# Optimization experiments

Measured on AMD Instinct MI355X. Metric: run time of the kernel, lower is better.

## Reference

```python
import jax, jax.numpy as jnp
import numpy as np

N = 100_000   # nodes
E = 1_600_000 # edges (avg degree 16)
D = 128       # in_dim
H = 128       # hidden_dim


def _glorot(key, shape):
    s = 1.0 / np.sqrt(shape[0])
    return jax.random.uniform(key, shape, jnp.float32, -s, s)


def setup_inputs() -> dict:
    key = jax.random.key(0)
    ks = jax.random.split(key, 8)
    x = jax.random.normal(ks[0], (N, D), jnp.float32)
    edge_index = jax.random.randint(ks[1], (2, E), 0, N)
    return {
        "x": x,
        "edge_index": edge_index,
        "Wn0": _glorot(ks[2], (D, H)),
        "Wr0": _glorot(ks[3], (D, H)),
        "b0": jnp.zeros((H,), jnp.float32),
        "Wn1": _glorot(ks[4], (H, H)),
        "Wr1": _glorot(ks[5], (H, H)),
        "b1": jnp.zeros((H,), jnp.float32),
        "Wh": _glorot(ks[6], (H, 1)),
        "bh": jnp.zeros((1,), jnp.float32),
    }


def _mean_agg(h, src, dst, n):
    # mean of source-node features scattered onto destination nodes
    summed = jax.ops.segment_sum(h[src], dst, num_segments=n)  # [N, F]
    cnt = jax.ops.segment_sum(jnp.ones((src.shape[0],), h.dtype), dst,
                              num_segments=n)
    return summed / jnp.maximum(cnt, 1.0)[:, None]


def _sage_layer(h, src, dst, Wn, Wr, b):
    # PyG SAGEConv (mean aggr): lin_l(mean_neighbors) + lin_r(root) + bias
    agg = _mean_agg(h, src, dst, h.shape[0])
    return agg @ Wn + h @ Wr + b


def reference(x, edge_index, Wn0, Wr0, b0, Wn1, Wr1, b1, Wh, bh):
    src, dst = edge_index[0], edge_index[1]
    h = jax.nn.relu(_sage_layer(x, src, dst, Wn0, Wr0, b0))  # dropout = identity (eval)
    h = jax.nn.relu(_sage_layer(h, src, dst, Wn1, Wr1, b1))
    logits = (h @ Wh + bh)[:, 0]  # squeeze(-1) -> [N]
    return logits
```

## Files before the change

### kernel.cpp

```cpp
#include <hip/hip_runtime.h>

#define THREADS 256
#define SCAN_ITEMS 8
#define NSB 128
#define BKT_MAX 3200
#define CHUNK 1024

typedef float f32x4 __attribute__((ext_vector_type(4)));
typedef __bf16 bf16x8 __attribute__((ext_vector_type(8)));
typedef int intx4 __attribute__((ext_vector_type(4)));

__device__ inline unsigned short f32_to_bf16_rne(float f) {
    unsigned int u = __float_as_uint(f);
    unsigned int r = u + 0x7fffu + ((u >> 16) & 1u);
    return (unsigned short)(r >> 16);
}
__device__ inline float bf16_bits_to_f32(unsigned short h) {
    return __uint_as_float(((unsigned int)h) << 16);
}
__device__ inline uint4 pack8(const unsigned short* s) {
    uint4 u;
    u.x = (unsigned int)s[0] | ((unsigned int)s[1] << 16);
    u.y = (unsigned int)s[2] | ((unsigned int)s[3] << 16);
    u.z = (unsigned int)s[4] | ((unsigned int)s[5] << 16);
    u.w = (unsigned int)s[6] | ((unsigned int)s[7] << 16);
    return u;
}

__global__ __launch_bounds__(256) void hist32(const int* __restrict__ dst,
                                              int* __restrict__ hist,
                                              int E, int nbkt, int chunk) {
    __shared__ int lh[BKT_MAX];
    const int tid = threadIdx.x, blk = blockIdx.x;
    for (int i = tid; i < nbkt; i += 256) lh[i] = 0;
    __syncthreads();
    int s = blk * chunk, e = s + chunk; if (e > E) e = E;
    if (((size_t)dst & 15) == 0) {
        int n4 = (e > s) ? ((e - s) >> 2) : 0;
        const intx4* d4p = (const intx4*)(dst + s);
        for (int i = tid; i < n4; i += 256) {
            intx4 d4 = d4p[i];
#pragma unroll
            for (int k = 0; k < 4; k++) atomicAdd(&lh[d4[k] >> 5], 1);
        }
        for (int j = s + (n4 << 2) + tid; j < e; j += 256) atomicAdd(&lh[dst[j] >> 5], 1);
    } else {
        for (int j = s + tid; j < e; j += 256) atomicAdd(&lh[dst[j] >> 5], 1);
    }
    __syncthreads();
    for (int i = tid; i < nbkt; i += 256) hist[i * NSB + blk] = lh[i];
}

__global__ void scan1_kernel(const int* __restrict__ cnt, int* __restrict__ off,
                             int* __restrict__ bsums, int n) {
    __shared__ int sdata[THREADS];
    int base = blockIdx.x * (THREADS * SCAN_ITEMS) + threadIdx.x * SCAN_ITEMS;
    int vals[SCAN_ITEMS];
    int tsum = 0;
#pragma unroll
    for (int k = 0; k < SCAN_ITEMS; k++) {
        int idx = base + k;
        int v = (idx < n) ? cnt[idx] : 0;
        vals[k] = tsum;
        tsum += v;
    }
    sdata[threadIdx.x] = tsum;
    __syncthreads();
    for (int s = 1; s < THREADS; s <<= 1) {
        int y = (threadIdx.x >= (unsigned)s) ? sdata[threadIdx.x - s] : 0;
        __syncthreads();
        sdata[threadIdx.x] += y;
        __syncthreads();
    }
    int texcl = sdata[threadIdx.x] - tsum;
#pragma unroll
    for (int k = 0; k < SCAN_ITEMS; k++) {
        int idx = base + k;
        if (idx < n) off[idx] = texcl + vals[k];
    }
    if (threadIdx.x == THREADS - 1) bsums[blockIdx.x] = sdata[THREADS - 1];
}

__global__ void scan2_kernel(const int* __restrict__ bsums, int* __restrict__ bbase,
                             int nb, int* __restrict__ offN) {
    if (threadIdx.x == 0 && blockIdx.x == 0) {
        int run = 0;
        for (int i = 0; i < nb; i++) { bbase[i] = run; run += bsums[i]; }
        *offN = run;
    }
}

__global__ void scan3b_kernel(int* __restrict__ off, const int* __restrict__ bbase, int n) {
    int i = blockIdx.x * blockDim.x + threadIdx.x;
    if (i < n) off[i] += bbase[i >> 11];
}

__global__ __launch_bounds__(256) void scatter32(const int* __restrict__ src,
                                                 const int* __restrict__ dst,
                                                 const int* __restrict__ hstS,
                                                 int* __restrict__ esrt,
                                                 int E, int nbkt, int chunk) {
    __shared__ int cur[BKT_MAX];
    const int tid = threadIdx.x, blk = blockIdx.x;
    for (int i = tid; i < nbkt; i += 256) cur[i] = hstS[i * NSB + blk];
    __syncthreads();
    int s = blk * chunk, e = s + chunk; if (e > E) e = E;
    if ((((size_t)dst | (size_t)src) & 15) == 0) {
        int n4 = (e > s) ? ((e - s) >> 2) : 0;
        const intx4* d4p = (const intx4*)(dst + s);
        const intx4* s4p = (const intx4*)(src + s);
        for (int i = tid; i < n4; i += 256) {
            intx4 d4 = d4p[i];
            intx4 s4 = s4p[i];
#pragma unroll
            for (int k = 0; k < 4; k++) {
                int d = d4[k];
                int p = atomicAdd(&cur[d >> 5], 1);
                esrt[p] = s4[k] | ((d & 31) << 17);
            }
        }
        for (int j = s + (n4 << 2) + tid; j < e; j += 256) {
            int d = dst[j];
            int p = atomicAdd(&cur[d >> 5], 1);
            esrt[p] = src[j] | ((d & 31) << 17);
        }
    } else {
        for (int j = s + tid; j < e; j += 256) {
            int d = dst[j];
            int p = atomicAdd(&cur[d >> 5], 1);
            esrt[p] = src[j] | ((d & 31) << 17);
        }
    }
}

__global__ void cvt_bf16_kernel(const float4* __restrict__ x, ushort4* __restrict__ o, int n4) {
    int i = blockIdx.x * blockDim.x + threadIdx.x;
    if (i < n4) {
        float4 v = x[i];
        ushort4 r;
        r.x = f32_to_bf16_rne(v.x);
        r.y = f32_to_bf16_rne(v.y);
        r.z = f32_to_bf16_rne(v.z);
        r.w = f32_to_bf16_rne(v.w);
        o[i] = r;
    }
}

__global__ void swizzle_w_kernel(const float* __restrict__ Wn, const float* __restrict__ Wr,
                                 uint4* __restrict__ out) {
    int id = blockIdx.x * blockDim.x + threadIdx.x;
    if (id >= 4096) return;
    int lane = id & 63;
    int nt = (id >> 6) & 7;
    int t = id >> 9;
    int kbase = t * 32 + (lane >> 4) * 8;
    int col = nt * 16 + (lane & 15);
    unsigned short hi[8], lo[8];
#pragma unroll
    for (int j = 0; j < 8; j++) {
        int k = kbase + j;
        const float* W = (k < 128) ? (Wn + (size_t)k * 128) : (Wr + (size_t)(k - 128) * 128);
        float v = W[col];
        unsigned short h = f32_to_bf16_rne(v);
        hi[j] = h;
        lo[j] = f32_to_bf16_rne(v - bf16_bits_to_f32(h));
    }
    out[(size_t)((t * 8 + nt) * 2 + 0) * 64 + lane] = pack8(hi);
    out[(size_t)((t * 8 + nt) * 2 + 1) * 64 + lane] = pack8(lo);
}

__global__ __launch_bounds__(256) void agg_bucket(const unsigned short* __restrict__ hb,
                                                  const int* __restrict__ hstS,
                                                  const int* __restrict__ esrt,
                                                  unsigned short* __restrict__ aggb,
                                                  int E, int nbkt, int n) {
    __shared__ int stage[CHUNK];
    __shared__ int sorted[CHUNK];
    __shared__ int cnt[32];
    __shared__ int coff[33];
    const int tid = threadIdx.x, lane = tid & 63, w = tid >> 6;
    const int b = blockIdx.x;

    const int p0 = hstS[b * NSB];
    const int p1 = (b + 1 < nbkt) ? hstS[(b + 1) * NSB] : E;

    if (p1 - p0 <= CHUNK) {
        int m = p1 - p0;
        for (int i = tid; i < m; i += 256) stage[i] = esrt[p0 + i];
        if (tid < 32) cnt[tid] = 0;
        __syncthreads();
        for (int i = tid; i < m; i += 256) atomicAdd(&cnt[(stage[i] >> 17) & 31], 1);
        __syncthreads();
        if (tid < 32) {
            int v = cnt[tid];
            int x = v;
#pragma unroll
            for (int s = 1; s < 32; s <<= 1) {
                int y = __shfl_up(x, s);
                if (lane >= s) x += y;
            }
            coff[tid + 1] = x;
            if (tid == 0) coff[0] = 0;
            cnt[tid] = x - v;
        }
        __syncthreads();
        for (int i = tid; i < m; i += 256) {
            int pk = stage[i];
            int p = atomicAdd(&cnt[(pk >> 17) & 31], 1);
            sorted[p] = pk;
        }
        __syncthreads();
        const int nodeEnd = w * 8 + 8;
        int cur = w * 8;
        int s = coff[cur], e2 = coff[nodeEnd];
        float ax = 0.f, ay = 0.f;
        int i = s;
        for (; i + 8 <= e2; i += 8) {
            unsigned int v[8];
            int nd[8];
#pragma unroll
            for (int j = 0; j < 8; j++) {
                int pk = sorted[i + j];
                nd[j] = (pk >> 17) & 31;
                v[j] = *(const unsigned int*)(hb + (size_t)(pk & 0x1FFFF) * 128 + lane * 2);
            }
#pragma unroll
            for (int j = 0; j < 8; j++) {
                while (cur < nd[j]) {
                    int node = b * 32 + cur;
                    int d = coff[cur + 1] - coff[cur];
                    float inv = 1.0f / (float)(d > 1 ? d : 1);
                    unsigned int o = (unsigned int)f32_to_bf16_rne(ax * inv)
                                   | ((unsigned int)f32_to_bf16_rne(ay * inv) << 16);
                    if (node < n)
                        *(unsigned int*)(aggb + (size_t)node * 128 + lane * 2) = o;
                    ax = 0.f; ay = 0.f; cur++;
                }
                ax += __uint_as_float(v[j] << 16);
                ay += __uint_as_float(v[j] & 0xffff0000u);
            }
        }
        for (; i < e2; i++) {
            int pk = sorted[i];
            int nd = (pk >> 17) & 31;
            unsigned int vv = *(const unsigned int*)(hb + (size_t)(pk & 0x1FFFF) * 128 + lane * 2);
            while (cur < nd) {
                int node = b * 32 + cur;
                int d = coff[cur + 1] - coff[cur];
                float inv = 1.0f / (float)(d > 1 ? d : 1);
                unsigned int o = (unsigned int)f32_to_bf16_rne(ax * inv)
                               | ((unsigned int)f32_to_bf16_rne(ay * inv) << 16);
                if (node < n)
                    *(unsigned int*)(aggb + (size_t)node * 128 + lane * 2) = o;
                ax = 0.f; ay = 0.f; cur++;
            }
            ax += __uint_as_float(vv << 16);
            ay += __uint_as_float(vv & 0xffff0000u);
        }
        while (cur < nodeEnd) {
            int node = b * 32 + cur;
            int d = coff[cur + 1] - coff[cur];
            float inv = 1.0f / (float)(d > 1 ? d : 1);
            unsigned int o = (unsigned int)f32_to_bf16_rne(ax * inv)
                           | ((unsigned int)f32_to_bf16_rne(ay * inv) << 16);
            if (node < n)
                *(unsigned int*)(aggb + (size_t)node * 128 + lane * 2) = o;
            ax = 0.f; ay = 0.f; cur++;
        }
        return;
    }

    float accx[8], accy[8];
    int dcnt[8];
#pragma unroll
    for (int nl = 0; nl < 8; nl++) { accx[nl] = 0.f; accy[nl] = 0.f; dcnt[nl] = 0; }
    for (int base = p0; base < p1; base += CHUNK) {
        int m = p1 - base; if (m > CHUNK) m = CHUNK;
        for (int i = tid; i < m; i += 256) stage[i] = esrt[base + i];
        if (tid < 32) cnt[tid] = 0;
        __syncthreads();
        for (int i = tid; i < m; i += 256) atomicAdd(&cnt[(stage[i] >> 17) & 31], 1);
        __syncthreads();
        if (tid < 32) {
            int v = cnt[tid];
            int x = v;
#pragma unroll
            for (int s = 1; s < 32; s <<= 1) {
                int y = __shfl_up(x, s);
                if (lane >= s) x += y;
            }
            coff[tid + 1] = x;
            if (tid == 0) coff[0] = 0;
            cnt[tid] = x - v;
        }
        __syncthreads();
        for (int i = tid; i < m; i += 256) {
            int pk = stage[i];
            int p = atomicAdd(&cnt[(pk >> 17) & 31], 1);
            sorted[p] = pk;
        }
        __syncthreads();
#pragma unroll
        for (int nl = 0; nl < 8; nl++) {
            int node_l = w * 8 + nl;
            int s = coff[node_l], e2 = coff[node_l + 1];
            dcnt[nl] += e2 - s;
            float ax = accx[nl], ay = accy[nl];
            int i = s;
            for (; i + 8 <= e2; i += 8) {
                unsigned int v[8];
#pragma unroll
                for (int j = 0; j < 8; j++) {
                    int sj = sorted[i + j] & 0x1FFFF;
                    v[j] = *(const unsigned int*)(hb + (size_t)sj * 128 + lane * 2);
                }
#pragma unroll
                for (int j = 0; j < 8; j++) {
                    ax += __uint_as_float(v[j] << 16);
                    ay += __uint_as_float(v[j] & 0xffff0000u);
                }
            }
            for (; i < e2; i++) {
                int sj = sorted[i] & 0x1FFFF;
                unsigned int vv = *(const unsigned int*)(hb + (size_t)sj * 128 + lane * 2);
                ax += __uint_as_float(vv << 16);
                ay += __uint_as_float(vv & 0xffff0000u);
            }
            accx[nl] = ax; accy[nl] = ay;
        }
        __syncthreads();
    }
#pragma unroll
    for (int nl = 0; nl < 8; nl++) {
        int node = b * 32 + w * 8 + nl;
        if (node < n) {
            int d = dcnt[nl];
            float inv = 1.0f / (float)(d > 1 ? d : 1);
            unsigned int o = (unsigned int)f32_to_bf16_rne(accx[nl] * inv)
                           | ((unsigned int)f32_to_bf16_rne(accy[nl] * inv) << 16);
            *(unsigned int*)(aggb + (size_t)node * 128 + lane * 2) = o;
        }
    }
}

template <int LAYER, bool FINAL>
__global__ __launch_bounds__(256, 2) void update_mfma(
    const unsigned short* __restrict__ aggb, const void* __restrict__ hsrc,
    const uint4* __restrict__ Wsw, const float* __restrict__ bias,
    unsigned short* __restrict__ hout,
    const float* __restrict__ Wh, const float* __restrict__ bh,
    float* __restrict__ logits, int n) {
    __shared__ uint4 Alds[2048];
    __shared__ uint4 Wlds[2048];
    const int tid = threadIdx.x;
    const int lane = tid & 63;
    const int w = tid >> 6;
    const int i0 = blockIdx.x * 128;

    f32x4 acc[2][8];
#pragma unroll
    for (int mt = 0; mt < 2; mt++)
#pragma unroll
        for (int nt = 0; nt < 8; nt++) acc[mt][nt] = (f32x4)0.f;

    const int r = tid >> 1;
    const int half = tid & 1;
    const int rg = i0 + r;
    const bool inb = rg < n;
    const int mt_s = r >> 4;
    const int lidx = r & 15;

    for (int c = 0; c < 4; c++) {
        const bool haslo = (LAYER == 0 && c >= 2);
        {
            const uint4* srcW = Wsw + (size_t)c * 2048;
#pragma unroll
            for (int g = 0; g < 8; g++) Wlds[g * 256 + tid] = srcW[g * 256 + tid];
        }
        {
            unsigned short hiA[32], loA[32];
            if (LAYER == 0 && c >= 2) {
                const float4* s4 = (const float4*)((const float*)hsrc + (size_t)rg * 128 +
                                                   (c - 2) * 64 + half * 32);
#pragma unroll
                for (int q = 0; q < 8; q++) {
                    float4 f = inb ? s4[q] : make_float4(0.f, 0.f, 0.f, 0.f);
                    float vv[4] = {f.x, f.y, f.z, f.w};
#pragma unroll
                    for (int e = 0; e < 4; e++) {
                        unsigned short h = f32_to_bf16_rne(vv[e]);
                        hiA[q * 4 + e] = h;
                        loA[q * 4 + e] = f32_to_bf16_rne(vv[e] - bf16_bits_to_f32(h));
                    }
                }
            } else {
                const unsigned short* bsrc = (c < 2) ? aggb : (const unsigned short*)hsrc;
                int cc = (c < 2) ? c : c - 2;
                const uint4* s4 = (const uint4*)(bsrc + (size_t)rg * 128 + cc * 64 + half * 32);
#pragma unroll
                for (int q = 0; q < 4; q++) {
                    uint4 u = inb ? s4[q] : make_uint4(0, 0, 0, 0);
                    unsigned int uu[4] = {u.x, u.y, u.z, u.w};
#pragma unroll
                    for (int e = 0; e < 4; e++) {
                        hiA[q * 8 + e * 2 + 0] = (unsigned short)(uu[e] & 0xffffu);
                        hiA[q * 8 + e * 2 + 1] = (unsigned short)(uu[e] >> 16);
                    }
                }
            }
            unsigned int baseHi = ((mt_s * 2 + half) * 2 + 0) * 64;
#pragma unroll
            for (int g2 = 0; g2 < 4; g2++)
                Alds[baseHi + lidx + 16 * g2] = pack8(&hiA[g2 * 8]);
            if (haslo) {
#pragma unroll
                for (int g2 = 0; g2 < 4; g2++)
                    Alds[baseHi + 64 + lidx + 16 * g2] = pack8(&loA[g2 * 8]);
            }
        }
        __syncthreads();
#pragma unroll
        for (int kt = 0; kt < 2; kt++) {
            bf16x8 a0h = *(const bf16x8*)&Alds[(((w * 2 + 0) * 2 + kt) * 2 + 0) * 64 + lane];
            bf16x8 a1h = *(const bf16x8*)&Alds[(((w * 2 + 1) * 2 + kt) * 2 + 0) * 64 + lane];
            bf16x8 a0l, a1l;
            if (haslo) {
                a0l = *(const bf16x8*)&Alds[(((w * 2 + 0) * 2 + kt) * 2 + 1) * 64 + lane];
                a1l = *(const bf16x8*)&Alds[(((w * 2 + 1) * 2 + kt) * 2 + 1) * 64 + lane];
            }
#pragma unroll
            for (int nt = 0; nt < 8; nt++) {
                bf16x8 bhv = *(const bf16x8*)&Wlds[((kt * 8 + nt) * 2 + 0) * 64 + lane];
                bf16x8 blv = *(const bf16x8*)&Wlds[((kt * 8 + nt) * 2 + 1) * 64 + lane];
                acc[0][nt] = __builtin_amdgcn_mfma_f32_16x16x32_bf16(a0h, bhv, acc[0][nt], 0, 0, 0);
                acc[0][nt] = __builtin_amdgcn_mfma_f32_16x16x32_bf16(a0h, blv, acc[0][nt], 0, 0, 0);
                acc[1][nt] = __builtin_amdgcn_mfma_f32_16x16x32_bf16(a1h, bhv, acc[1][nt], 0, 0, 0);
                acc[1][nt] = __builtin_amdgcn_mfma_f32_16x16x32_bf16(a1h, blv, acc[1][nt], 0, 0, 0);
                if (haslo) {
                    acc[0][nt] = __builtin_amdgcn_mfma_f32_16x16x32_bf16(a0l, bhv, acc[0][nt], 0, 0, 0);
                    acc[1][nt] = __builtin_amdgcn_mfma_f32_16x16x32_bf16(a1l, bhv, acc[1][nt], 0, 0, 0);
                }
            }
        }
        __syncthreads();
    }

    const int col = lane & 15;
    const int g4 = lane >> 4;
    float bcol[8];
#pragma unroll
    for (int nt = 0; nt < 8; nt++) bcol[nt] = bias[nt * 16 + col];
    if (!FINAL) {
#pragma unroll
        for (int mt = 0; mt < 2; mt++) {
            int nodeBase = i0 + (w * 2 + mt) * 16 + g4 * 4;
#pragma unroll
            for (int reg = 0; reg < 4; reg++) {
                int node = nodeBase + reg;
                if (node < n) {
#pragma unroll
                    for (int nt = 0; nt < 8; nt++) {
                        float v = acc[mt][nt][reg] + bcol[nt];
                        v = v > 0.f ? v : 0.f;
                        hout[(size_t)node * 128 + nt * 16 + col] = f32_to_bf16_rne(v);
                    }
                }
            }
        }
    } else {
        float whc[8];
#pragma unroll
        for (int nt = 0; nt < 8; nt++) whc[nt] = Wh[nt * 16 + col];
        float bhv = bh[0];
#pragma unroll
        for (int mt = 0; mt < 2; mt++) {
            int nodeBase = i0 + (w * 2 + mt) * 16 + g4 * 4;
#pragma unroll
            for (int reg = 0; reg < 4; reg++) {
                float s = 0.f;
#pragma unroll
                for (int nt = 0; nt < 8; nt++) {
                    float v = acc[mt][nt][reg] + bcol[nt];
                    v = v > 0.f ? v : 0.f;
                    s += v * whc[nt];
                }
                s += __shfl_xor(s, 1);
                s += __shfl_xor(s, 2);
                s += __shfl_xor(s, 4);
                s += __shfl_xor(s, 8);
                int node = nodeBase + reg;
                if (col == 0 && node < n) logits[node] = s + bhv;
            }
        }
    }
}

extern "C" void kernel_launch(void* const* d_in, const int* in_sizes, int n_in,
                              void* d_out, int out_size, void* d_ws, size_t ws_size,
                              hipStream_t stream) {
    const float* x   = (const float*)d_in[0];
    const int*   ei  = (const int*)d_in[1];
    const float* Wn0 = (const float*)d_in[2];
    const float* Wr0 = (const float*)d_in[3];
    const float* b0  = (const float*)d_in[4];
    const float* Wn1 = (const float*)d_in[5];
    const float* Wr1 = (const float*)d_in[6];
    const float* b1  = (const float*)d_in[7];
    const float* Wh  = (const float*)d_in[8];
    const float* bh  = (const float*)d_in[9];
    float* logits = (float*)d_out;

    int N = in_sizes[0] / 128;
    int E = in_sizes[1] / 2;
    const int* src = ei;
    const int* dst = ei + E;

    int nbkt = (N + 31) >> 5;
    int HS = nbkt * NSB;
    int NB = (HS + 2047) / 2048;
    int chunk = (((E + NSB - 1) / NSB) + 3) & ~3;

    char* ws = (char*)d_ws;
    size_t cur = 0;
    auto alloc = [&](size_t bytes) -> void* {
        void* p = ws + cur;
        cur += (bytes + 255) & ~(size_t)255;
        return p;
    };
    int* hist  = (int*)alloc((size_t)HS * 4);
    int* bsums = (int*)alloc((size_t)NB * 4);
    int* bbase = (int*)alloc((size_t)NB * 4);
    int* scrat = (int*)alloc(256);
    int* esrt  = (int*)alloc((size_t)E * 4);
    unsigned short* xb  = (unsigned short*)alloc((size_t)N * 128 * 2);
    unsigned short* h0b = (unsigned short*)alloc((size_t)N * 128 * 2);
    unsigned short* agb = (unsigned short*)alloc((size_t)N * 128 * 2);
    uint4* Wsw0 = (uint4*)alloc(131072);
    uint4* Wsw1 = (uint4*)alloc(131072);
    (void)ws_size; (void)n_in; (void)out_size;

    int n4 = N * 32;
    hipLaunchKernelGGL(cvt_bf16_kernel, dim3((n4 + 255) / 256), dim3(256), 0, stream,
                       (const float4*)x, (ushort4*)xb, n4);
    hipLaunchKernelGGL(swizzle_w_kernel, dim3(16), dim3(256), 0, stream, Wn0, Wr0, Wsw0);
    hipLaunchKernelGGL(swizzle_w_kernel, dim3(16), dim3(256), 0, stream, Wn1, Wr1, Wsw1);

    hipLaunchKernelGGL(hist32,        dim3(NSB), dim3(256), 0, stream, dst, hist, E, nbkt, chunk);
    hipLaunchKernelGGL(scan1_kernel,  dim3(NB),  dim3(256), 0, stream, hist, hist, bsums, HS);
    hipLaunchKernelGGL(scan2_kernel,  dim3(1),   dim3(64),  0, stream, bsums, bbase, NB, scrat);
    hipLaunchKernelGGL(scan3b_kernel, dim3((HS + 255) / 256), dim3(256), 0, stream, hist, bbase, HS);
    hipLaunchKernelGGL(scatter32,     dim3(NSB), dim3(256), 0, stream, src, dst, hist, esrt, E, nbkt, chunk);

    int gUpd = (N + 127) / 128;

    hipLaunchKernelGGL(agg_bucket, dim3(nbkt), dim3(256), 0, stream, xb, hist, esrt, agb, E, nbkt, N);
    hipLaunchKernelGGL((update_mfma<0, false>), dim3(gUpd), dim3(256), 0, stream,
                       agb, (const void*)x, Wsw0, b0, h0b, nullptr, nullptr, nullptr, N);
    hipLaunchKernelGGL(agg_bucket, dim3(nbkt), dim3(256), 0, stream, h0b, hist, esrt, agb, E, nbkt, N);
    hipLaunchKernelGGL((update_mfma<1, true>), dim3(gUpd), dim3(256), 0, stream,
                       agb, (const void*)h0b, Wsw1, b1, nullptr, Wh, bh, logits, N);
}
```

Baseline: 355.4 us.

## Precompute per-node sorted edge list once and simplify aggregation with pipelined gathers

Adds a sort2 kernel that performs the per-bucket counting sort by destination once, writing a fully node-sorted edge array and per-node offsets (CSR). Both aggregation layers now read this global CSR directly instead of re-sorting in LDS each time, removing the shared-memory staging, barriers and the large-bucket fallback path. The gather loop is software-pipelined with double-buffered batches of eight loads to overlap memory latency. In exchange it adds an extra kernel launch, extra global memory traffic for the second edge array, and global reads of offsets.

```diff
diff --git a/kernel.cpp b/kernel.cpp
--- a/kernel.cpp
+++ b/kernel.cpp
@@ -4,11 +4,12 @@
 #define SCAN_ITEMS 8
 #define NSB 128
 #define BKT_MAX 3200
-#define CHUNK 1024
 
 typedef float f32x4 __attribute__((ext_vector_type(4)));
 typedef __bf16 bf16x8 __attribute__((ext_vector_type(8)));
 typedef int intx4 __attribute__((ext_vector_type(4)));
+typedef int intx8 __attribute__((ext_vector_type(8)));
+typedef unsigned int uintx8 __attribute__((ext_vector_type(8)));
 
 __device__ inline unsigned short f32_to_bf16_rne(float f) {
     unsigned int u = __float_as_uint(f);
@@ -130,6 +131,42 @@
             int p = atomicAdd(&cur[d >> 5], 1);
             esrt[p] = src[j] | ((d & 31) << 17);
         }
+    }
+}
+
+__global__ __launch_bounds__(256) void sort2(const int* __restrict__ esrt,
+                                             const int* __restrict__ hstS,
+                                             int* __restrict__ esrt2,
+                                             int* __restrict__ noff,
+                                             int E, int nbkt) {
+    __shared__ int cnt[32];
+    __shared__ int cur[32];
+    const int tid = threadIdx.x;
+    const int b = blockIdx.x;
+    const int p0 = hstS[b * NSB];
+    const int p1 = (b + 1 < nbkt) ? hstS[(b + 1) * NSB] : E;
+    if (tid < 32) cnt[tid] = 0;
+    __syncthreads();
+    for (int i = p0 + tid; i < p1; i += 256) atomicAdd(&cnt[(esrt[i] >> 17) & 31], 1);
+    __syncthreads();
+    if (tid < 32) {
+        int v = cnt[tid];
+        int x = v;
+#pragma unroll
+        for (int s = 1; s < 32; s <<= 1) {
+            int y = __shfl_up(x, s);
+            if ((tid & 63) >= s) x += y;
+        }
+        int excl = x - v;
+        cur[tid] = p0 + excl;
+        noff[b * 32 + tid] = p0 + excl;
+    }
+    if (tid == 0 && b == 0) noff[nbkt * 32] = E;
+    __syncthreads();
+    for (int i = p0 + tid; i < p1; i += 256) {
+        int pk = esrt[i];
+        int p = atomicAdd(&cur[(pk >> 17) & 31], 1);
+        esrt2[p] = pk;
     }
 }
 
@@ -169,178 +206,80 @@
     out[(size_t)((t * 8 + nt) * 2 + 1) * 64 + lane] = pack8(lo);
 }
 
-__global__ __launch_bounds__(256) void agg_bucket(const unsigned short* __restrict__ hb,
-                                                  const int* __restrict__ hstS,
-                                                  const int* __restrict__ esrt,
+__global__ __launch_bounds__(256) void agg_gather(const unsigned short* __restrict__ hb,
+                                                  const int* __restrict__ esrt2,
+                                                  const int* __restrict__ noff,
                                                   unsigned short* __restrict__ aggb,
-                                                  int E, int nbkt, int n) {
-    __shared__ int stage[CHUNK];
-    __shared__ int sorted[CHUNK];
-    __shared__ int cnt[32];
-    __shared__ int coff[33];
-    const int tid = threadIdx.x, lane = tid & 63, w = tid >> 6;
-    const int b = blockIdx.x;
-
-    const int p0 = hstS[b * NSB];
-    const int p1 = (b + 1 < nbkt) ? hstS[(b + 1) * NSB] : E;
-
-    if (p1 - p0 <= CHUNK) {
-        int m = p1 - p0;
-        for (int i = tid; i < m; i += 256) stage[i] = esrt[p0 + i];
-        if (tid < 32) cnt[tid] = 0;
-        __syncthreads();
-        for (int i = tid; i < m; i += 256) atomicAdd(&cnt[(stage[i] >> 17) & 31], 1);
-        __syncthreads();
-        if (tid < 32) {
-            int v = cnt[tid];
-            int x = v;
-#pragma unroll
-            for (int s = 1; s < 32; s <<= 1) {
-                int y = __shfl_up(x, s);
-                if (lane >= s) x += y;
-            }
-            coff[tid + 1] = x;
-            if (tid == 0) coff[0] = 0;
-            cnt[tid] = x - v;
-        }
-        __syncthreads();
-        for (int i = tid; i < m; i += 256) {
-            int pk = stage[i];
-            int p = atomicAdd(&cnt[(pk >> 17) & 31], 1);
-            sorted[p] = pk;
-        }
-        __syncthreads();
-        const int nodeEnd = w * 8 + 8;
-        int cur = w * 8;
-        int s = coff[cur], e2 = coff[nodeEnd];
-        float ax = 0.f, ay = 0.f;
-        int i = s;
-        for (; i + 8 <= e2; i += 8) {
-            unsigned int v[8];
-            int nd[8];
-#pragma unroll
-            for (int j = 0; j < 8; j++) {
-                int pk = sorted[i + j];
-                nd[j] = (pk >> 17) & 31;
-                v[j] = *(const unsigned int*)(hb + (size_t)(pk & 0x1FFFF) * 128 + lane * 2);
-            }
-#pragma unroll
-            for (int j = 0; j < 8; j++) {
-                while (cur < nd[j]) {
-                    int node = b * 32 + cur;
-                    int d = coff[cur + 1] - coff[cur];
-                    float inv = 1.0f / (float)(d > 1 ? d : 1);
-                    unsigned int o = (unsigned int)f32_to_bf16_rne(ax * inv)
-                                   | ((unsigned int)f32_to_bf16_rne(ay * inv) << 16);
-                    if (node < n)
-                        *(unsigned int*)(aggb + (size_t)node * 128 + lane * 2) = o;
-                    ax = 0.f; ay = 0.f; cur++;
-                }
-                ax += __uint_as_float(v[j] << 16);
-                ay += __uint_as_float(v[j] & 0xffff0000u);
-            }
-        }
-        for (; i < e2; i++) {
-            int pk = sorted[i];
-            int nd = (pk >> 17) & 31;
-            unsigned int vv = *(const unsigned int*)(hb + (size_t)(pk & 0x1FFFF) * 128 + lane * 2);
-            while (cur < nd) {
-                int node = b * 32 + cur;
-                int d = coff[cur + 1] - coff[cur];
-                float inv = 1.0f / (float)(d > 1 ? d : 1);
-                unsigned int o = (unsigned int)f32_to_bf16_rne(ax * inv)
-                               | ((unsigned int)f32_to_bf16_rne(ay * inv) << 16);
-                if (node < n)
-                    *(unsigned int*)(aggb + (size_t)node * 128 + lane * 2) = o;
-                ax = 0.f; ay = 0.f; cur++;
-            }
-            ax += __uint_as_float(vv << 16);
-            ay += __uint_as_float(vv & 0xffff0000u);
-        }
-        while (cur < nodeEnd) {
-            int node = b * 32 + cur;
-            int d = coff[cur + 1] - coff[cur];
+                                                  int n, int nTot) {
+    const int tid = threadIdx.x, lane = tid & 63;
+    const int w4 = __builtin_amdgcn_readfirstlane(tid >> 6);
+    const int bucketBase = blockIdx.x * 32;
+    const int node0 = bucketBase + w4 * 8;
+    if (node0 >= nTot) return;
+    const int nodeEndL = w4 * 8 + 8;
+    int cur = w4 * 8;
+    const int s = noff[node0];
+    const int e2 = noff[node0 + 8];
+
+    float ax = 0.f, ay = 0.f;
+
+    auto flushTo = [&](int tgt) {
+        while (cur < tgt) {
+            int node = bucketBase + cur;
+            int d = noff[node + 1] - noff[node];
             float inv = 1.0f / (float)(d > 1 ? d : 1);
             unsigned int o = (unsigned int)f32_to_bf16_rne(ax * inv)
                            | ((unsigned int)f32_to_bf16_rne(ay * inv) << 16);
             if (node < n)
                 *(unsigned int*)(aggb + (size_t)node * 128 + lane * 2) = o;
-            ax = 0.f; ay = 0.f; cur++;
-        }
-        return;
-    }
-
-    float accx[8], accy[8];
-    int dcnt[8];
-#pragma unroll
-    for (int nl = 0; nl < 8; nl++) { accx[nl] = 0.f; accy[nl] = 0.f; dcnt[nl] = 0; }
-    for (int base = p0; base < p1; base += CHUNK) {
-        int m = p1 - base; if (m > CHUNK) m = CHUNK;
-        for (int i = tid; i < m; i += 256) stage[i] = esrt[base + i];
-        if (tid < 32) cnt[tid] = 0;
-        __syncthreads();
-        for (int i = tid; i < m; i += 256) atomicAdd(&cnt[(stage[i] >> 17) & 31], 1);
-        __syncthreads();
-        if (tid < 32) {
-            int v = cnt[tid];
-            int x = v;
-#pragma unroll
-            for (int s = 1; s < 32; s <<= 1) {
-                int y = __shfl_up(x, s);
-                if (lane >= s) x += y;
-            }
-            coff[tid + 1] = x;
-            if (tid == 0) coff[0] = 0;
-            cnt[tid] = x - v;
-        }
-        __syncthreads();
-        for (int i = tid; i < m; i += 256) {
-            int pk = stage[i];
-            int p = atomicAdd(&cnt[(pk >> 17) & 31], 1);
-            sorted[p] = pk;
-        }
-        __syncthreads();
-#pragma unroll
-        for (int nl = 0; nl < 8; nl++) {
-            int node_l = w * 8 + nl;
-            int s = coff[node_l], e2 = coff[node_l + 1];
-            dcnt[nl] += e2 - s;
-            float ax = accx[nl], ay = accy[nl];
-            int i = s;
-            for (; i + 8 <= e2; i += 8) {
-                unsigned int v[8];
-#pragma unroll
-                for (int j = 0; j < 8; j++) {
-                    int sj = sorted[i + j] & 0x1FFFF;
-                    v[j] = *(const unsigned int*)(hb + (size_t)sj * 128 + lane * 2);
-                }
-#pragma unroll
-                for (int j = 0; j < 8; j++) {
-                    ax += __uint_as_float(v[j] << 16);
-                    ay += __uint_as_float(v[j] & 0xffff0000u);
-                }
-            }
-            for (; i < e2; i++) {
-                int sj = sorted[i] & 0x1FFFF;
-                unsigned int vv = *(const unsigned int*)(hb + (size_t)sj * 128 + lane * 2);
-                ax += __uint_as_float(vv << 16);
-                ay += __uint_as_float(vv & 0xffff0000u);
-            }
-            accx[nl] = ax; accy[nl] = ay;
-        }
-        __syncthreads();
-    }
-#pragma unroll
-    for (int nl = 0; nl < 8; nl++) {
-        int node = b * 32 + w * 8 + nl;
-        if (node < n) {
-            int d = dcnt[nl];
-            float inv = 1.0f / (float)(d > 1 ? d : 1);
-            unsigned int o = (unsigned int)f32_to_bf16_rne(accx[nl] * inv)
-                           | ((unsigned int)f32_to_bf16_rne(accy[nl] * inv) << 16);
-            *(unsigned int*)(aggb + (size_t)node * 128 + lane * 2) = o;
-        }
-    }
+            ax = 0.f; ay = 0.f; ++cur;
+        }
+    };
+    auto issue = [&](uintx8& V, intx8& ND, int base) {
+#pragma unroll
+        for (int j = 0; j < 8; j++) {
+            int pk = esrt2[base + j];
+            ND[j] = (pk >> 17) & 31;
+            V[j] = *(const unsigned int*)(hb + (size_t)(pk & 0x1FFFF) * 128 + lane * 2);
+        }
+    };
+    auto consume = [&](const uintx8& V, const intx8& ND) {
+#pragma unroll
+        for (int j = 0; j < 8; j++) {
+            flushTo(ND[j]);
+            ax += __uint_as_float(V[j] << 16);
+            ay += __uint_as_float(V[j] & 0xffff0000u);
+        }
+    };
+
+    const int nbch = (e2 - s) >> 3;
+    uintx8 vA, vB;
+    intx8 ndA, ndB;
+    if (nbch > 0) {
+        issue(vA, ndA, s);
+        int k = 1;
+        for (; k + 1 < nbch; k += 2) {
+            issue(vB, ndB, s + k * 8);
+            consume(vA, ndA);
+            issue(vA, ndA, s + k * 8 + 8);
+            consume(vB, ndB);
+        }
+        if (k < nbch) {
+            issue(vB, ndB, s + k * 8);
+            consume(vA, ndA);
+            consume(vB, ndB);
+        } else {
+            consume(vA, ndA);
+        }
+    }
+    for (int i = s + (nbch << 3); i < e2; i++) {
+        int pk = esrt2[i];
+        flushTo((pk >> 17) & 31);
+        unsigned int vv = *(const unsigned int*)(hb + (size_t)(pk & 0x1FFFF) * 128 + lane * 2);
+        ax += __uint_as_float(vv << 16);
+        ay += __uint_as_float(vv & 0xffff0000u);
+    }
+    flushTo(nodeEndL);
 }
 
 template <int LAYER, bool FINAL>
@@ -516,6 +455,7 @@
     const int* dst = ei + E;
 
     int nbkt = (N + 31) >> 5;
+    int nTot = nbkt * 32;
     int HS = nbkt * NSB;
     int NB = (HS + 2047) / 2048;
     int chunk = (((E + NSB - 1) / NSB) + 3) & ~3;
@@ -532,6 +472,8 @@
     int* bbase = (int*)alloc((size_t)NB * 4);
     int* scrat = (int*)alloc(256);
     int* esrt  = (int*)alloc((size_t)E * 4);
+    int* esrt2 = (int*)alloc((size_t)E * 4);
+    int* noff  = (int*)alloc((size_t)(nTot + 1) * 4);
     unsigned short* xb  = (unsigned short*)alloc((size_t)N * 128 * 2);
     unsigned short* h0b = (unsigned short*)alloc((size_t)N * 128 * 2);
     unsigned short* agb = (unsigned short*)alloc((size_t)N * 128 * 2);
@@ -550,13 +492,14 @@
     hipLaunchKernelGGL(scan2_kernel,  dim3(1),   dim3(64),  0, stream, bsums, bbase, NB, scrat);
     hipLaunchKernelGGL(scan3b_kernel, dim3((HS + 255) / 256), dim3(256), 0, stream, hist, bbase, HS);
     hipLaunchKernelGGL(scatter32,     dim3(NSB), dim3(256), 0, stream, src, dst, hist, esrt, E, nbkt, chunk);
+    hipLaunchKernelGGL(sort2,         dim3(nbkt), dim3(256), 0, stream, esrt, hist, esrt2, noff, E, nbkt);
 
     int gUpd = (N + 127) / 128;
 
-    hipLaunchKernelGGL(agg_bucket, dim3(nbkt), dim3(256), 0, stream, xb, hist, esrt, agb, E, nbkt, N);
+    hipLaunchKernelGGL(agg_gather, dim3(nbkt), dim3(256), 0, stream, xb, esrt2, noff, agb, N, nTot);
     hipLaunchKernelGGL((update_mfma<0, false>), dim3(gUpd), dim3(256), 0, stream,
                        agb, (const void*)x, Wsw0, b0, h0b, nullptr, nullptr, nullptr, N);
-    hipLaunchKernelGGL(agg_bucket, dim3(nbkt), dim3(256), 0, stream, h0b, hist, esrt, agb, E, nbkt, N);
+    hipLaunchKernelGGL(agg_gather, dim3(nbkt), dim3(256), 0, stream, h0b, esrt2, noff, agb, N, nTot);
     hipLaunchKernelGGL((update_mfma<1, true>), dim3(gUpd), dim3(256), 0, stream,
                        agb, (const void*)h0b, Wsw1, b1, nullptr, Wh, bh, logits, N);
 }
```

Measured after the change: 374.4 us. +5.4%, slower.

## Double-buffer gathers in bucket aggregation, parallelize block scan, double histogram blocks

Applied to the files above, without the earlier changes.

The per-wave aggregation loop now issues the next batch of eight neighbour-row gathers before accumulating the current batch (A/B double buffering), and keeps node offsets in registers instead of rereading LDS. This is meant to hide global-memory gather latency. The single-thread serial scan of block sums is replaced by a wave-wide shuffle scan. The number of histogram/scatter blocks doubles from 128 to 256, which changes the hist layout size and chunking and increases register pressure.

```diff
diff --git a/kernel.cpp b/kernel.cpp
--- a/kernel.cpp
+++ b/kernel.cpp
@@ -2,7 +2,7 @@
 
 #define THREADS 256
 #define SCAN_ITEMS 8
-#define NSB 128
+#define NSB 256
 #define BKT_MAX 3200
 #define CHUNK 1024
 
@@ -81,13 +81,23 @@
     if (threadIdx.x == THREADS - 1) bsums[blockIdx.x] = sdata[THREADS - 1];
 }
 
-__global__ void scan2_kernel(const int* __restrict__ bsums, int* __restrict__ bbase,
-                             int nb, int* __restrict__ offN) {
-    if (threadIdx.x == 0 && blockIdx.x == 0) {
-        int run = 0;
-        for (int i = 0; i < nb; i++) { bbase[i] = run; run += bsums[i]; }
-        *offN = run;
-    }
+__global__ void scan2_wave(const int* __restrict__ bsums, int* __restrict__ bbase,
+                           int nb, int* __restrict__ offN) {
+    const int lane = threadIdx.x;
+    int carry = 0;
+    for (int base = 0; base < nb; base += 64) {
+        int i = base + lane;
+        int v = (i < nb) ? bsums[i] : 0;
+        int x = v;
+#pragma unroll
+        for (int s = 1; s < 64; s <<= 1) {
+            int y = __shfl_up(x, s);
+            if (lane >= s) x += y;
+        }
+        if (i < nb) bbase[i] = carry + x - v;
+        carry += __shfl(x, 63);
+    }
+    if (lane == 0) *offN = carry;
 }
 
 __global__ void scan3b_kernel(int* __restrict__ off, const int* __restrict__ bbase, int n) {
@@ -210,63 +220,71 @@
             sorted[p] = pk;
         }
         __syncthreads();
-        const int nodeEnd = w * 8 + 8;
-        int cur = w * 8;
-        int s = coff[cur], e2 = coff[nodeEnd];
+
+        int no[9];
+#pragma unroll
+        for (int i = 0; i <= 8; i++) no[i] = coff[w * 8 + i];
+        const int s = no[0], e2 = no[8];
+        int curL = 0;
         float ax = 0.f, ay = 0.f;
-        int i = s;
-        for (; i + 8 <= e2; i += 8) {
-            unsigned int v[8];
-            int nd[8];
-#pragma unroll
-            for (int j = 0; j < 8; j++) {
-                int pk = sorted[i + j];
-                nd[j] = (pk >> 17) & 31;
-                v[j] = *(const unsigned int*)(hb + (size_t)(pk & 0x1FFFF) * 128 + lane * 2);
-            }
-#pragma unroll
-            for (int j = 0; j < 8; j++) {
-                while (cur < nd[j]) {
-                    int node = b * 32 + cur;
-                    int d = coff[cur + 1] - coff[cur];
-                    float inv = 1.0f / (float)(d > 1 ? d : 1);
-                    unsigned int o = (unsigned int)f32_to_bf16_rne(ax * inv)
-                                   | ((unsigned int)f32_to_bf16_rne(ay * inv) << 16);
-                    if (node < n)
-                        *(unsigned int*)(aggb + (size_t)node * 128 + lane * 2) = o;
-                    ax = 0.f; ay = 0.f; cur++;
-                }
-                ax += __uint_as_float(v[j] << 16);
-                ay += __uint_as_float(v[j] & 0xffff0000u);
-            }
-        }
-        for (; i < e2; i++) {
-            int pk = sorted[i];
-            int nd = (pk >> 17) & 31;
-            unsigned int vv = *(const unsigned int*)(hb + (size_t)(pk & 0x1FFFF) * 128 + lane * 2);
-            while (cur < nd) {
-                int node = b * 32 + cur;
-                int d = coff[cur + 1] - coff[cur];
+
+        auto flushTo = [&](int tgt) {
+            while (curL < tgt) {
+                int node = b * 32 + w * 8 + curL;
+                int d = no[curL + 1] - no[curL];
                 float inv = 1.0f / (float)(d > 1 ? d : 1);
                 unsigned int o = (unsigned int)f32_to_bf16_rne(ax * inv)
                                | ((unsigned int)f32_to_bf16_rne(ay * inv) << 16);
                 if (node < n)
                     *(unsigned int*)(aggb + (size_t)node * 128 + lane * 2) = o;
-                ax = 0.f; ay = 0.f; cur++;
-            }
+                ax = 0.f; ay = 0.f; ++curL;
+            }
+        };
+        auto issue = [&](unsigned int* v, int* nd, int base) {
+#pragma unroll
+            for (int j = 0; j < 8; j++) {
+                int pk = sorted[base + j];
+                nd[j] = ((pk >> 17) & 31) - w * 8;
+                v[j] = *(const unsigned int*)(hb + (size_t)(pk & 0x1FFFF) * 128 + lane * 2);
+            }
+        };
+        auto consume = [&](const unsigned int* v, const int* nd) {
+#pragma unroll
+            for (int j = 0; j < 8; j++) {
+                flushTo(nd[j]);
+                ax += __uint_as_float(v[j] << 16);
+                ay += __uint_as_float(v[j] & 0xffff0000u);
+            }
+        };
+
+        const int nb8 = (e2 - s) >> 3;
+        unsigned int vA[8], vB[8];
+        int ndA[8], ndB[8];
+        if (nb8 > 0) {
+            issue(vA, ndA, s);
+            int k = 1;
+            for (; k + 1 < nb8; k += 2) {
+                issue(vB, ndB, s + k * 8);
+                consume(vA, ndA);
+                issue(vA, ndA, s + k * 8 + 8);
+                consume(vB, ndB);
+            }
+            if (k < nb8) {
+                issue(vB, ndB, s + k * 8);
+                consume(vA, ndA);
+                consume(vB, ndB);
+            } else {
+                consume(vA, ndA);
+            }
+        }
+        for (int i = s + (nb8 << 3); i < e2; i++) {
+            int pk = sorted[i];
+            flushTo(((pk >> 17) & 31) - w * 8);
+            unsigned int vv = *(const unsigned int*)(hb + (size_t)(pk & 0x1FFFF) * 128 + lane * 2);
             ax += __uint_as_float(vv << 16);
             ay += __uint_as_float(vv & 0xffff0000u);
         }
-        while (cur < nodeEnd) {
-            int node = b * 32 + cur;
-            int d = coff[cur + 1] - coff[cur];
-            float inv = 1.0f / (float)(d > 1 ? d : 1);
-            unsigned int o = (unsigned int)f32_to_bf16_rne(ax * inv)
-                           | ((unsigned int)f32_to_bf16_rne(ay * inv) << 16);
-            if (node < n)
-                *(unsigned int*)(aggb + (size_t)node * 128 + lane * 2) = o;
-            ax = 0.f; ay = 0.f; cur++;
-        }
+        flushTo(8);
         return;
     }
 
@@ -547,7 +565,7 @@
 
     hipLaunchKernelGGL(hist32,        dim3(NSB), dim3(256), 0, stream, dst, hist, E, nbkt, chunk);
     hipLaunchKernelGGL(scan1_kernel,  dim3(NB),  dim3(256), 0, stream, hist, hist, bsums, HS);
-    hipLaunchKernelGGL(scan2_kernel,  dim3(1),   dim3(64),  0, stream, bsums, bbase, NB, scrat);
+    hipLaunchKernelGGL(scan2_wave,    dim3(1),   dim3(64),  0, stream, bsums, bbase, NB, scrat);
     hipLaunchKernelGGL(scan3b_kernel, dim3((HS + 255) / 256), dim3(256), 0, stream, hist, bbase, HS);
     hipLaunchKernelGGL(scatter32,     dim3(NSB), dim3(256), 0, stream, src, dst, hist, esrt, E, nbkt, chunk);
 
```

After: 362.2 us. About the same (+1.9%).
